# Performance work log

Hardware: AMD Instinct MI355X
Metric: run time of the kernel (lower is better)

The kernel has to match this reference:

```python
import jax, jax.numpy as jnp
import numpy as np

B, S, D, H = 256, 128, 1024, 8
DH = D // H  # per-head dim = input_length / head


def setup_inputs() -> dict:
    key = jax.random.key(0)
    ks = jax.random.split(key, 12)
    code = jax.random.normal(ks[0], (B, S, D), dtype=jnp.float32)
    # 0/1 adjacency (PDG relation mask)
    input_relation = jax.random.bernoulli(ks[1], 0.2, (B, S, S)).astype(jnp.float32)
    w = 0.02
    Wq = jax.random.normal(ks[2], (H, D, DH), dtype=jnp.float32) * w
    bq = jnp.zeros((H, DH), dtype=jnp.float32)
    Wk = jax.random.normal(ks[3], (H, D, DH), dtype=jnp.float32) * w
    bk = jnp.zeros((H, DH), dtype=jnp.float32)
    Wv = jax.random.normal(ks[4], (H, D, DH), dtype=jnp.float32) * w
    bv = jnp.zeros((H, DH), dtype=jnp.float32)
    Wo = jax.random.normal(ks[5], (2 * D, D), dtype=jnp.float32) * w
    bo = jnp.zeros((D,), dtype=jnp.float32)
    return {"code": code, "input_relation": input_relation,
            "Wq": Wq, "bq": bq, "Wk": Wk, "bk": bk,
            "Wv": Wv, "bv": bv, "Wo": Wo, "bo": bo}


def reference(code, input_relation, Wq, bq, Wk, bk, Wv, bv, Wo, bo):
    Hn = Wq.shape[0]
    half = Hn // 2
    Sn = code.shape[1]
    E = jnp.eye(Sn, dtype=code.dtype)
    # Faithful to the TF loop: head i < H/2 sees relation + i*I (the loop
    # reassigns input_relation = this_relation + I each iteration);
    # heads i >= H/2 see the ORIGINAL transposed relation.
    i_idx = jnp.arange(half, dtype=code.dtype)  # [half]
    rel_fwd = input_relation[None] + i_idx[:, None, None, None] * E  # [half,B,S,S]
    rel_t = jnp.swapaxes(input_relation, 1, 2)
    rel_bwd = jnp.broadcast_to(rel_t[None], (Hn - half,) + rel_t.shape)
    rels = jnp.concatenate([rel_fwd, rel_bwd], axis=0)  # [H,B,S,S]

    relu = jax.nn.relu
    Q = relu(jnp.einsum('bsd,hdf->hbsf', code, Wq) + bq[:, None, None, :])
    K = relu(jnp.einsum('bsd,hdf->hbsf', code, Wk) + bk[:, None, None, :])
    V = relu(jnp.einsum('bsd,hdf->hbsf', code, Wv) + bv[:, None, None, :])

    attn = jnp.einsum('hbsf,hbtf->hbst', Q, K)  # [H,B,S,S]
    pdg = rels * attn + 1e-11
    # tf.reduce_sum axis=1 (rows) -> our axis=2; axis=2 (cols) -> our axis=3
    indeg = jnp.sqrt(jnp.sum(pdg, axis=2, keepdims=True))   # [H,B,1,S]
    outdeg = jnp.sqrt(jnp.sum(pdg, axis=3, keepdims=True))  # [H,B,S,1]
    pdg = pdg / indeg / outdeg
    softed = rels * pdg
    res = jnp.einsum('hbst,hbtf->hbsf', softed, V)  # [H,B,S,DH]

    # concat heads along features (head 0 first), then concat original code
    all_ch = jnp.transpose(res, (1, 2, 0, 3)).reshape(code.shape[0], Sn, -1)
    add_ori = jnp.concatenate([all_ch, code], axis=-1)  # [B,S,2D]
    out = relu(add_ori @ Wo + bo)
    return out
```

## Files before the change

### kernel.cpp

```cpp
#include <hip/hip_runtime.h>
#include <cstdint>
#include <cstddef>

#define B_  256
#define S_  128
#define D_  1024
#define H_  8
#define DH_ 128
#define M_  (B_ * S_)

typedef _Float16 half8 __attribute__((ext_vector_type(8)));
typedef float    f32x4 __attribute__((ext_vector_type(4)));

#define GLOAD_LDS16(gp, lp)                                                    \
    __builtin_amdgcn_global_load_lds(                                          \
        (const __attribute__((address_space(1))) void*)(gp),                   \
        (__attribute__((address_space(3))) void*)(lp), 16, 0, 0)

__global__ __launch_bounds__(256)
void cvt_code(const float* __restrict__ src, _Float16* __restrict__ dst, int n8)
{
    int i = blockIdx.x * 256 + threadIdx.x;
    if (i >= n8) return;
    const float4* s = (const float4*)src;
    float4 a = s[2 * i], b = s[2 * i + 1];
    half8 o;
    o[0] = (_Float16)a.x; o[1] = (_Float16)a.y; o[2] = (_Float16)a.z; o[3] = (_Float16)a.w;
    o[4] = (_Float16)b.x; o[5] = (_Float16)b.y; o[6] = (_Float16)b.z; o[7] = (_Float16)b.w;
    *(half8*)(dst + (size_t)i * 8) = o;
}

__global__ __launch_bounds__(256)
void cvt_wqkv(const float* __restrict__ Wq, const float* __restrict__ Wk,
              const float* __restrict__ Wv,
              const float* __restrict__ bq, const float* __restrict__ bk,
              const float* __restrict__ bv,
              _Float16* __restrict__ Wt, float* __restrict__ bias_all)
{
    int idx = blockIdx.x * 256 + threadIdx.x;
    if (idx >= 3072 * 128) return;
    int n = idx >> 7, kc = idx & 127, k = kc * 8;
    int qkv = n >> 10, hf = n & 1023, h = hf >> 7, f = hf & 127;
    const float* W = (qkv == 0 ? Wq : (qkv == 1 ? Wk : Wv))
                     + (size_t)h * D_ * DH_ + (size_t)k * DH_ + f;
    half8 o;
    #pragma unroll
    for (int j = 0; j < 8; ++j) o[j] = (_Float16)W[(size_t)j * DH_];
    *(half8*)(Wt + (size_t)n * 1024 + k) = o;
    if (kc == 0)
        bias_all[n] = (qkv == 0 ? bq : (qkv == 1 ? bk : bv))[h * DH_ + f];
}

__global__ __launch_bounds__(256)
void cvt_wo(const float* __restrict__ Wo, _Float16* __restrict__ Wot)
{
    int idx = blockIdx.x * 256 + threadIdx.x;
    if (idx >= 1024 * 256) return;
    int n = idx >> 8, kc = idx & 255, k = kc * 8;
    const float* W = Wo + (size_t)k * 1024 + n;
    half8 o;
    #pragma unroll
    for (int j = 0; j < 8; ++j) o[j] = (_Float16)W[(size_t)j * 1024];
    *(half8*)(Wot + (size_t)n * 2048 + k) = o;
}

template <bool OUTF32>
__global__ __launch_bounds__(512, 1)
void gemm_f16_8p(const _Float16* __restrict__ A1p, const _Float16* __restrict__ A2p,
                 int K1, const _Float16* __restrict__ Bt,
                 const float* __restrict__ bias, void* __restrict__ outp,
                 int Ntot, int Ktot, int ntn)
{
    __shared__ __align__(16) char lds[131072];

    const int tid = threadIdx.x;
    const int w = tid >> 6, l = tid & 63;
    const int wm = w >> 2, wn = w & 3;
    const int lr = l & 15, lg = l >> 4;

    const int cpx = gridDim.x >> 3;
    const int bid = blockIdx.x;
    const int swz = (bid & 7) * cpx + (bid >> 3);
    const int m0 = (swz / ntn) * 256, n0 = (swz % ntn) * 256;

    const int NT = Ktot >> 6;

    const int srow  = l >> 3;
    const int sgcol = ((l & 7) ^ srow) * 8;

    auto stageHalf = [&](int bufi, int t, int half) {
        const int k0 = t << 6;
        const bool isA = (half == 0) || (half == 3);
        const int hh = (half >= 2) ? 1 : 0;
        char* dst0 = lds + bufi * 65536 + (isA ? 0 : 32768) + hh * 16384;
        if (isA) {
            const _Float16* Asrc; int kc;
            if (k0 < K1) { Asrc = A1p; kc = k0; } else { Asrc = A2p; kc = k0 - K1; }
            #pragma unroll
            for (int i = 0; i < 2; ++i) {
                const int c = i * 8 + w;
                const int row = hh * 128 + c * 8 + srow;
                const _Float16* g = Asrc + (size_t)(m0 + row) * 1024 + kc + sgcol;
                GLOAD_LDS16(g, dst0 + c * 1024);
            }
        } else {
            #pragma unroll
            for (int i = 0; i < 2; ++i) {
                const int c = i * 8 + w;
                const int row = hh * 128 + c * 8 + srow;
                const _Float16* g = Bt + (size_t)(n0 + row) * Ktot + k0 + sgcol;
                GLOAD_LDS16(g, dst0 + c * 1024);
            }
        }
    };

    auto ldA = [&](int bufi, int fi, int ks) -> half8 {
        const int row = fi * 32 + wm * 16 + lr;
        const int pos = (ks * 4 + lg) ^ (row & 7);
        return *(const half8*)(lds + bufi * 65536 + row * 128 + pos * 16);
    };
    auto ldB = [&](int bufi, int fj, int ks) -> half8 {
        const int row = fj * 64 + wn * 16 + lr;
        const int pos = (ks * 4 + lg) ^ (row & 7);
        return *(const half8*)(lds + bufi * 65536 + 32768 + row * 128 + pos * 16);
    };

    f32x4 acc[8][4] = {};
    half8 aq[4][2], b0[2][2], b1[2][2];

    stageHalf(0, 0, 0); stageHalf(0, 0, 1); stageHalf(0, 0, 2); stageHalf(0, 0, 3);

    for (int t = 0; t < NT; ++t) {
        const int buf = t & 1;
        const bool nl = (t + 1 < NT);

        asm volatile("s_waitcnt vmcnt(4)" ::: "memory");
        __builtin_amdgcn_s_barrier();
        #pragma unroll
        for (int fi = 0; fi < 4; ++fi)
            #pragma unroll
            for (int ks = 0; ks < 2; ++ks)
                aq[fi][ks] = ldA(buf, fi, ks);
        #pragma unroll
        for (int fj = 0; fj < 2; ++fj)
            #pragma unroll
            for (int ks = 0; ks < 2; ++ks)
                b0[fj][ks] = ldB(buf, fj, ks);
        if (nl) stageHalf(buf ^ 1, t + 1, 0);
        asm volatile("s_waitcnt lgkmcnt(0)" ::: "memory");
        __builtin_amdgcn_sched_barrier(0);
        __builtin_amdgcn_s_setprio(1);
        #pragma unroll
        for (int ks = 0; ks < 2; ++ks)
            #pragma unroll
            for (int fi = 0; fi < 4; ++fi)
                #pragma unroll
                for (int fj = 0; fj < 2; ++fj)
                    acc[fi][fj] = __builtin_amdgcn_mfma_f32_16x16x32_f16(
                        aq[fi][ks], b0[fj][ks], acc[fi][fj], 0, 0, 0);
        __builtin_amdgcn_s_setprio(0);
        __builtin_amdgcn_s_barrier();

        if (nl) asm volatile("s_waitcnt vmcnt(4)" ::: "memory");
        else    asm volatile("s_waitcnt vmcnt(2)" ::: "memory");
        __builtin_amdgcn_s_barrier();
        #pragma unroll
        for (int fj = 0; fj < 2; ++fj)
            #pragma unroll
            for (int ks = 0; ks < 2; ++ks)
                b1[fj][ks] = ldB(buf, fj + 2, ks);
        if (nl) stageHalf(buf ^ 1, t + 1, 1);
        asm volatile("s_waitcnt lgkmcnt(0)" ::: "memory");
        __builtin_amdgcn_sched_barrier(0);
        __builtin_amdgcn_s_setprio(1);
        #pragma unroll
        for (int ks = 0; ks < 2; ++ks)
            #pragma unroll
            for (int fi = 0; fi < 4; ++fi)
                #pragma unroll
                for (int fj = 0; fj < 2; ++fj)
                    acc[fi][fj + 2] = __builtin_amdgcn_mfma_f32_16x16x32_f16(
                        aq[fi][ks], b1[fj][ks], acc[fi][fj + 2], 0, 0, 0);
        __builtin_amdgcn_s_setprio(0);
        __builtin_amdgcn_s_barrier();

        if (nl) asm volatile("s_waitcnt vmcnt(4)" ::: "memory");
        else    asm volatile("s_waitcnt vmcnt(0)" ::: "memory");
        __builtin_amdgcn_s_barrier();
        #pragma unroll
        for (int fi = 0; fi < 4; ++fi)
            #pragma unroll
            for (int ks = 0; ks < 2; ++ks)
                aq[fi][ks] = ldA(buf, fi + 4, ks);
        if (nl) stageHalf(buf ^ 1, t + 1, 2);
        asm volatile("s_waitcnt lgkmcnt(0)" ::: "memory");
        __builtin_amdgcn_sched_barrier(0);
        __builtin_amdgcn_s_setprio(1);
        #pragma unroll
        for (int ks = 0; ks < 2; ++ks)
            #pragma unroll
            for (int fi = 0; fi < 4; ++fi)
                #pragma unroll
                for (int fj = 0; fj < 2; ++fj)
                    acc[fi + 4][fj + 2] = __builtin_amdgcn_mfma_f32_16x16x32_f16(
                        aq[fi][ks], b1[fj][ks], acc[fi + 4][fj + 2], 0, 0, 0);
        __builtin_amdgcn_s_setprio(0);
        __builtin_amdgcn_s_barrier();

        if (nl) stageHalf(buf ^ 1, t + 1, 3);
        __builtin_amdgcn_s_setprio(1);
        #pragma unroll
        for (int ks = 0; ks < 2; ++ks)
            #pragma unroll
            for (int fi = 0; fi < 4; ++fi)
                #pragma unroll
                for (int fj = 0; fj < 2; ++fj)
                    acc[fi + 4][fj] = __builtin_amdgcn_mfma_f32_16x16x32_f16(
                        aq[fi][ks], b0[fj][ks], acc[fi + 4][fj], 0, 0, 0);
        __builtin_amdgcn_s_setprio(0);
        __builtin_amdgcn_s_barrier();
    }

    #pragma unroll
    for (int fi = 0; fi < 8; ++fi) {
        #pragma unroll
        for (int fj = 0; fj < 4; ++fj) {
            const int n = n0 + fj * 64 + wn * 16 + lr;
            const float bs = bias[n];
            #pragma unroll
            for (int rg = 0; rg < 4; ++rg) {
                const int m = m0 + fi * 32 + wm * 16 + lg * 4 + rg;
                float v = acc[fi][fj][rg] + bs;
                v = v > 0.0f ? v : 0.0f;
                if constexpr (OUTF32)
                    ((float*)outp)[(size_t)m * Ntot + n] = v;
                else
                    ((_Float16*)outp)[(size_t)m * Ntot + n] = (_Float16)v;
            }
        }
    }
}

#define PPAD 136
#define VPAD 40

__global__ __launch_bounds__(256, 2)
void attn_pdg_mfma(const _Float16* __restrict__ QKV, const float* __restrict__ Rel,
                   _Float16* __restrict__ resh)
{
    __shared__ __align__(16) char smem[72704];
    _Float16* P     = (_Float16*)smem;
    _Float16* Qs    = (_Float16*)(smem + 34816);
    _Float16* Ks    = Qs + 2 * 4096;
    _Float16* Vt    = (_Float16*)(smem + 34816);
    unsigned* rbits = (unsigned*)(smem + 67584);
    float* rowpart  = (float*)(smem + 69632);
    float* colpart  = (float*)(smem + 70656);
    float* inv_in   = (float*)(smem + 71680);
    float* inv_out  = (float*)(smem + 72192);

    const int tid = threadIdx.x;
    const int w = tid >> 6, l = tid & 63;
    const int wr = w >> 1, wc = w & 1;
    const int lr = l & 15, lg = l >> 4;
    const int b = blockIdx.x, h = blockIdx.y;

    for (int s = w; s < S_; s += 4) {
        const float* row = &Rel[((size_t)b * S_ + s) * S_];
        unsigned long long b0 = __ballot(row[l] > 0.5f);
        unsigned long long b1 = __ballot(row[64 + l] > 0.5f);
        if (l == 0) {
            rbits[s * 4 + 0] = (unsigned)b0; rbits[s * 4 + 1] = (unsigned)(b0 >> 32);
            rbits[s * 4 + 2] = (unsigned)b1; rbits[s * 4 + 3] = (unsigned)(b1 >> 32);
        }
    }

    const size_t gbase = (size_t)(b * S_) * 3072 + h * DH_;

    auto stageQK = [&](int bufi, int t) {
        const int k0 = t * 32;
        const int rr = l >> 2, cc = (l & 3) * 8;
        #pragma unroll
        for (int i = 0; i < 2; ++i) {
            const int row = w * 32 + i * 16;
            const _Float16* gq = QKV + gbase + (size_t)(row + rr) * 3072 + k0 + cc;
            GLOAD_LDS16(gq, Qs + bufi * 4096 + row * 32);
            const _Float16* gk = QKV + gbase + 1024 + (size_t)(row + rr) * 3072 + k0 + cc;
            GLOAD_LDS16(gk, Ks + bufi * 4096 + row * 32);
        }
    };

    f32x4 acc[4][4] = {};
    stageQK(0, 0);
    __syncthreads();
    int buf = 0;
    for (int t = 0; t < 4; ++t) {
        if (t < 3) stageQK(buf ^ 1, t + 1);
        half8 af[4], bf[4];
        #pragma unroll
        for (int i = 0; i < 4; ++i)
            af[i] = *(const half8*)&Qs[buf * 4096 + (wr * 64 + i * 16 + lr) * 32 + lg * 8];
        #pragma unroll
        for (int j = 0; j < 4; ++j)
            bf[j] = *(const half8*)&Ks[buf * 4096 + (wc * 64 + j * 16 + lr) * 32 + lg * 8];
        #pragma unroll
        for (int i = 0; i < 4; ++i)
            #pragma unroll
            for (int j = 0; j < 4; ++j)
                acc[i][j] = __builtin_amdgcn_mfma_f32_16x16x32_f16(af[i], bf[j], acc[i][j], 0, 0, 0);
        __syncthreads();
        buf ^= 1;
    }

    auto relf = [&](int s, int t) -> float {
        float r;
        if (h < H_ / 2) {
            r = (float)((rbits[s * 4 + (t >> 5)] >> (t & 31)) & 1u);
            if (s == t) r += (float)h;
        } else {
            r = (float)((rbits[t * 4 + (s >> 5)] >> (s & 31)) & 1u);
        }
        return r;
    };

    f32x4 p[4][4];
    #pragma unroll
    for (int i = 0; i < 4; ++i)
        #pragma unroll
        for (int j = 0; j < 4; ++j)
            #pragma unroll
            for (int rg = 0; rg < 4; ++rg) {
                const int s = wr * 64 + i * 16 + lg * 4 + rg;
                const int t = wc * 64 + j * 16 + lr;
                p[i][j][rg] = relf(s, t) * acc[i][j][rg] + 1e-11f;
            }

    #pragma unroll
    for (int i = 0; i < 4; ++i)
        #pragma unroll
        for (int rg = 0; rg < 4; ++rg) {
            float part = p[i][0][rg] + p[i][1][rg] + p[i][2][rg] + p[i][3][rg];
            part += __shfl_xor(part, 1);
            part += __shfl_xor(part, 2);
            part += __shfl_xor(part, 4);
            part += __shfl_xor(part, 8);
            if (lr == 0) rowpart[wc * 128 + wr * 64 + i * 16 + lg * 4 + rg] = part;
        }
    #pragma unroll
    for (int j = 0; j < 4; ++j) {
        float part = 0.0f;
        #pragma unroll
        for (int i = 0; i < 4; ++i)
            part += p[i][j][0] + p[i][j][1] + p[i][j][2] + p[i][j][3];
        part += __shfl_xor(part, 16);
        part += __shfl_xor(part, 32);
        if (lg == 0) colpart[wr * 128 + wc * 64 + j * 16 + lr] = part;
    }
    __syncthreads();

    if (tid < 128) {
        inv_in[tid] = rsqrtf(colpart[tid] + colpart[128 + tid]);
    } else {
        const int s = tid - 128;
        inv_out[s] = rsqrtf(rowpart[s] + rowpart[128 + s]);
    }
    __syncthreads();

    float itj[4];
    #pragma unroll
    for (int j = 0; j < 4; ++j) itj[j] = inv_in[wc * 64 + j * 16 + lr];
    #pragma unroll
    for (int i = 0; i < 4; ++i)
        #pragma unroll
        for (int rg = 0; rg < 4; ++rg) {
            const int s = wr * 64 + i * 16 + lg * 4 + rg;
            const float os = inv_out[s];
            #pragma unroll
            for (int j = 0; j < 4; ++j) {
                const int t = wc * 64 + j * 16 + lr;
                const float val = relf(s, t) * p[i][j][rg] * itj[j] * os;
                P[s * PPAD + t] = (_Float16)val;
            }
        }

    const _Float16* Vb = QKV + gbase + 2048;
    uint4 vreg[2];
    auto loadV = [&](int t) {
        #pragma unroll
        for (int ii = 0; ii < 2; ++ii) {
            const int unit = tid + ii * 256;
            const int tt = unit & 31, fg = unit >> 5;
            vreg[ii] = *(const uint4*)&Vb[(size_t)(t * 32 + tt) * 3072 + fg * 8];
        }
    };

    loadV(0);
    f32x4 acc2[4][4] = {};
    for (int t = 0; t < 4; ++t) {
        #pragma unroll
        for (int ii = 0; ii < 2; ++ii) {
            union { uint4 u; _Float16 hh[8]; } uu;
            uu.u = vreg[ii];
            const int unit = tid + ii * 256;
            const int tt = unit & 31, fg = unit >> 5;
            #pragma unroll
            for (int e = 0; e < 8; ++e)
                Vt[(fg * 8 + e) * VPAD + tt] = uu.hh[e];
        }
        __syncthreads();
        if (t < 3) loadV(t + 1);

        half8 af[4], bf[4];
        #pragma unroll
        for (int i = 0; i < 4; ++i)
            af[i] = *(const half8*)&P[(wr * 64 + i * 16 + lr) * PPAD + t * 32 + lg * 8];
        #pragma unroll
        for (int j = 0; j < 4; ++j)
            bf[j] = *(const half8*)&Vt[(wc * 64 + j * 16 + lr) * VPAD + lg * 8];
        #pragma unroll
        for (int i = 0; i < 4; ++i)
            #pragma unroll
            for (int j = 0; j < 4; ++j)
                acc2[i][j] = __builtin_amdgcn_mfma_f32_16x16x32_f16(af[i], bf[j], acc2[i][j], 0, 0, 0);
        __syncthreads();
    }

    #pragma unroll
    for (int i = 0; i < 4; ++i)
        #pragma unroll
        for (int rg = 0; rg < 4; ++rg) {
            const int s = wr * 64 + i * 16 + lg * 4 + rg;
            #pragma unroll
            for (int j = 0; j < 4; ++j) {
                const int f = wc * 64 + j * 16 + lr;
                resh[((size_t)(b * S_ + s)) * 1024 + h * DH_ + f] = (_Float16)acc2[i][j][rg];
            }
        }
}

extern "C" void kernel_launch(void* const* d_in, const int* in_sizes, int n_in,
                              void* d_out, int out_size, void* d_ws, size_t ws_size,
                              hipStream_t stream)
{
    const float* code = (const float*)d_in[0];
    const float* Rel  = (const float*)d_in[1];
    const float* Wq   = (const float*)d_in[2];
    const float* bq   = (const float*)d_in[3];
    const float* Wk   = (const float*)d_in[4];
    const float* bk   = (const float*)d_in[5];
    const float* Wv   = (const float*)d_in[6];
    const float* bv   = (const float*)d_in[7];
    const float* Wo   = (const float*)d_in[8];
    const float* bo   = (const float*)d_in[9];
    float* out = (float*)d_out;
    (void)in_sizes; (void)n_in; (void)out_size; (void)ws_size;

    char* wsp = (char*)d_ws;
    _Float16* codeh = (_Float16*)wsp;  wsp += (size_t)M_ * 1024 * 2;
    _Float16* QKV   = (_Float16*)wsp;  wsp += (size_t)M_ * 3072 * 2;
    _Float16* resh  = (_Float16*)wsp;  wsp += (size_t)M_ * 1024 * 2;
    _Float16* Wt    = (_Float16*)wsp;  wsp += (size_t)3072 * 1024 * 2;
    _Float16* Wot   = (_Float16*)wsp;  wsp += (size_t)1024 * 2048 * 2;
    float* bias_all = (float*)wsp;     wsp += 3072 * 4;

    cvt_code<<<(M_ * 1024 / 8 + 255) / 256, 256, 0, stream>>>(code, codeh, M_ * 1024 / 8);
    cvt_wqkv<<<(3072 * 128 + 255) / 256, 256, 0, stream>>>(Wq, Wk, Wv, bq, bk, bv, Wt, bias_all);
    cvt_wo<<<(1024 * 256 + 255) / 256, 256, 0, stream>>>(Wo, Wot);

    gemm_f16_8p<false><<<(M_ / 256) * (3072 / 256), 512, 0, stream>>>(
        codeh, codeh, 1024, Wt, bias_all, (void*)QKV, 3072, 1024, 3072 / 256);

    attn_pdg_mfma<<<dim3(B_, H_), 256, 0, stream>>>(QKV, Rel, resh);

    gemm_f16_8p<true><<<(M_ / 256) * (1024 / 256), 512, 0, stream>>>(
        resh, codeh, 1024, Wot, bo, (void*)out, 1024, 2048, 1024 / 256);
}
```

Measured before the change: 568.1 us.

## Software-pipeline LDS fragment reads to overlap with MFMA in GEMM main loop

Restructures the 4-phase GEMM inner loop so LDS fragment loads for the next phase are issued before the current phase's MFMAs and waited with partial lgkmcnt counts. A second A-fragment register set is added, and the next tile's first fragments are preloaded at the end of each iteration. The aim is to hide LDS read latency behind matrix math. In exchange it raises register pressure and changes the barrier and wait ordering, which risks hazards or lower occupancy.

```diff
diff --git a/kernel.cpp b/kernel.cpp
--- a/kernel.cpp
+++ b/kernel.cpp
@@ -126,28 +126,39 @@
     };
 
     f32x4 acc[8][4] = {};
-    half8 aq[4][2], b0[2][2], b1[2][2];
+    half8 aqA[4][2], aqB[4][2], b0[2][2], b1[2][2];
 
     stageHalf(0, 0, 0); stageHalf(0, 0, 1); stageHalf(0, 0, 2); stageHalf(0, 0, 3);
+    asm volatile("s_waitcnt vmcnt(4)" ::: "memory");
+    __builtin_amdgcn_s_barrier();
+    #pragma unroll
+    for (int fi = 0; fi < 4; ++fi)
+        #pragma unroll
+        for (int ks = 0; ks < 2; ++ks)
+            aqA[fi][ks] = ldA(0, fi, ks);
+    #pragma unroll
+    for (int fj = 0; fj < 2; ++fj)
+        #pragma unroll
+        for (int ks = 0; ks < 2; ++ks)
+            b0[fj][ks] = ldB(0, fj, ks);
 
     for (int t = 0; t < NT; ++t) {
         const int buf = t & 1;
         const bool nl = (t + 1 < NT);
 
-        asm volatile("s_waitcnt vmcnt(4)" ::: "memory");
-        __builtin_amdgcn_s_barrier();
-        #pragma unroll
-        for (int fi = 0; fi < 4; ++fi)
+        if (nl) {
+            stageHalf(buf ^ 1, t + 1, 0);
+            asm volatile("s_waitcnt vmcnt(4)" ::: "memory");
+        } else {
+            asm volatile("s_waitcnt vmcnt(2)" ::: "memory");
+        }
+        __builtin_amdgcn_s_barrier();
+        #pragma unroll
+        for (int fj = 0; fj < 2; ++fj)
             #pragma unroll
             for (int ks = 0; ks < 2; ++ks)
-                aq[fi][ks] = ldA(buf, fi, ks);
-        #pragma unroll
-        for (int fj = 0; fj < 2; ++fj)
-            #pragma unroll
-            for (int ks = 0; ks < 2; ++ks)
-                b0[fj][ks] = ldB(buf, fj, ks);
-        if (nl) stageHalf(buf ^ 1, t + 1, 0);
-        asm volatile("s_waitcnt lgkmcnt(0)" ::: "memory");
+                b1[fj][ks] = ldB(buf, fj + 2, ks);
+        asm volatile("s_waitcnt lgkmcnt(4)" ::: "memory");
         __builtin_amdgcn_sched_barrier(0);
         __builtin_amdgcn_s_setprio(1);
         #pragma unroll
@@ -157,20 +168,23 @@
                 #pragma unroll
                 for (int fj = 0; fj < 2; ++fj)
                     acc[fi][fj] = __builtin_amdgcn_mfma_f32_16x16x32_f16(
-                        aq[fi][ks], b0[fj][ks], acc[fi][fj], 0, 0, 0);
+                        aqA[fi][ks], b0[fj][ks], acc[fi][fj], 0, 0, 0);
         __builtin_amdgcn_s_setprio(0);
         __builtin_amdgcn_s_barrier();
 
-        if (nl) asm volatile("s_waitcnt vmcnt(4)" ::: "memory");
-        else    asm volatile("s_waitcnt vmcnt(2)" ::: "memory");
-        __builtin_amdgcn_s_barrier();
-        #pragma unroll
-        for (int fj = 0; fj < 2; ++fj)
+        if (nl) {
+            stageHalf(buf ^ 1, t + 1, 1);
+            asm volatile("s_waitcnt vmcnt(4)" ::: "memory");
+        } else {
+            asm volatile("s_waitcnt vmcnt(0)" ::: "memory");
+        }
+        __builtin_amdgcn_s_barrier();
+        #pragma unroll
+        for (int fi = 0; fi < 4; ++fi)
             #pragma unroll
             for (int ks = 0; ks < 2; ++ks)
-                b1[fj][ks] = ldB(buf, fj + 2, ks);
-        if (nl) stageHalf(buf ^ 1, t + 1, 1);
-        asm volatile("s_waitcnt lgkmcnt(0)" ::: "memory");
+                aqB[fi][ks] = ldA(buf, fi + 4, ks);
+        asm volatile("s_waitcnt lgkmcnt(8)" ::: "memory");
         __builtin_amdgcn_sched_barrier(0);
         __builtin_amdgcn_s_setprio(1);
         #pragma unroll
@@ -180,20 +194,18 @@
                 #pragma unroll
                 for (int fj = 0; fj < 2; ++fj)
                     acc[fi][fj + 2] = __builtin_amdgcn_mfma_f32_16x16x32_f16(
-                        aq[fi][ks], b1[fj][ks], acc[fi][fj + 2], 0, 0, 0);
+                        aqA[fi][ks], b1[fj][ks], acc[fi][fj + 2], 0, 0, 0);
         __builtin_amdgcn_s_setprio(0);
         __builtin_amdgcn_s_barrier();
 
-        if (nl) asm volatile("s_waitcnt vmcnt(4)" ::: "memory");
-        else    asm volatile("s_waitcnt vmcnt(0)" ::: "memory");
-        __builtin_amdgcn_s_barrier();
-        #pragma unroll
-        for (int fi = 0; fi < 4; ++fi)
+        if (nl) stageHalf(buf ^ 1, t + 1, 2);
+        __builtin_amdgcn_s_barrier();
+        #pragma unroll
+        for (int fj = 0; fj < 2; ++fj)
             #pragma unroll
             for (int ks = 0; ks < 2; ++ks)
-                aq[fi][ks] = ldA(buf, fi + 4, ks);
-        if (nl) stageHalf(buf ^ 1, t + 1, 2);
-        asm volatile("s_waitcnt lgkmcnt(0)" ::: "memory");
+                b0[fj][ks] = ldB(buf, fj, ks);
+        asm volatile("s_waitcnt lgkmcnt(4)" ::: "memory");
         __builtin_amdgcn_sched_barrier(0);
         __builtin_amdgcn_s_setprio(1);
         #pragma unroll
@@ -203,11 +215,17 @@
                 #pragma unroll
                 for (int fj = 0; fj < 2; ++fj)
                     acc[fi + 4][fj + 2] = __builtin_amdgcn_mfma_f32_16x16x32_f16(
-                        aq[fi][ks], b1[fj][ks], acc[fi + 4][fj + 2], 0, 0, 0);
+                        aqB[fi][ks], b1[fj][ks], acc[fi + 4][fj + 2], 0, 0, 0);
         __builtin_amdgcn_s_setprio(0);
         __builtin_amdgcn_s_barrier();
 
-        if (nl) stageHalf(buf ^ 1, t + 1, 3);
+        if (nl) {
+            stageHalf(buf ^ 1, t + 1, 3);
+            asm volatile("s_waitcnt vmcnt(4)" ::: "memory");
+        }
+        __builtin_amdgcn_s_barrier();
+        asm volatile("s_waitcnt lgkmcnt(0)" ::: "memory");
+        __builtin_amdgcn_sched_barrier(0);
         __builtin_amdgcn_s_setprio(1);
         #pragma unroll
         for (int ks = 0; ks < 2; ++ks)
@@ -216,8 +234,20 @@
                 #pragma unroll
                 for (int fj = 0; fj < 2; ++fj)
                     acc[fi + 4][fj] = __builtin_amdgcn_mfma_f32_16x16x32_f16(
-                        aq[fi][ks], b0[fj][ks], acc[fi + 4][fj], 0, 0, 0);
+                        aqB[fi][ks], b0[fj][ks], acc[fi + 4][fj], 0, 0, 0);
         __builtin_amdgcn_s_setprio(0);
+        if (nl) {
+            #pragma unroll
+            for (int fi = 0; fi < 4; ++fi)
+                #pragma unroll
+                for (int ks = 0; ks < 2; ++ks)
+                    aqA[fi][ks] = ldA(buf ^ 1, fi, ks);
+            #pragma unroll
+            for (int fj = 0; fj < 2; ++fj)
+                #pragma unroll
+                for (int ks = 0; ks < 2; ++ks)
+                    b0[fj][ks] = ldB(buf ^ 1, fj, ks);
+        }
         __builtin_amdgcn_s_barrier();
     }
 
```

Measured after the change: 583.3 us. +2.7%, slower.
